# Performance work log

Hardware: AMD Instinct MI355X
Metric: run time of the kernel (lower is better)

## Reference

```python
import jax, jax.numpy as jnp
import numpy as np

E, D, H, B, S = 16, 1024, 256, 4, 4096  # num_splats, model_dim, ff_dim//num_splats, batch, seq_len


def setup_inputs() -> dict:
    key = jax.random.key(0)
    ks = jax.random.split(key, 8)
    s = 0.02  # init scale for stability
    return {
        "x": jax.random.normal(ks[0], (B, S, D), dtype=jnp.float32),
        "splat_id": jax.random.randint(ks[1], (S,), 0, E, dtype=jnp.int32),
        "W1": jax.random.normal(ks[2], (E, D, H), dtype=jnp.float32) * s,
        "b1": jnp.zeros((E, H), dtype=jnp.float32),
        "W2": jax.random.normal(ks[3], (E, H, D), dtype=jnp.float32) * s,
        "b2": jnp.zeros((E, D), dtype=jnp.float32),
        "Wg1": jax.random.normal(ks[4], (D, D), dtype=jnp.float32) * s,
        "bg1": jnp.zeros((D,), dtype=jnp.float32),
        "Wg2": jax.random.normal(ks[5], (D, D), dtype=jnp.float32) * s,
        "bg2": jnp.zeros((D,), dtype=jnp.float32),
    }


def reference(x, splat_id, W1, b1, W2, b2, Wg1, bg1, Wg2, bg2):
    # Splat-aware dispatch: token s is processed by expert splat_id[s].
    # Equivalent vectorized form: run every expert's small MLP, mask at the
    # hidden layer by expert assignment, and sum over experts (each token is
    # assigned to exactly one expert, matching the gather->MLP->scatter loop).
    nE = W1.shape[0]
    onehot = (splat_id[None, :] == jnp.arange(nE, dtype=splat_id.dtype)[:, None]).astype(x.dtype)  # [E,S]
    # hidden: [E,B,S,H]
    h = jax.nn.gelu(jnp.einsum('bsd,edh->ebsh', x, W1) + b1[:, None, None, :], approximate=False)
    h = h * onehot[:, None, :, None]  # zero tokens not routed to expert e
    routed = jnp.einsum('ebsh,ehd->bsd', h, W2)  # [B,S,D]
    routed = routed + jnp.einsum('es,ed->sd', onehot, b2)[None, :, :]  # per-token expert bias
    # global aggregator MLP (torch GELU default = exact erf form)
    g = jax.nn.gelu(routed @ Wg1 + bg1, approximate=False)
    return g @ Wg2 + bg2
```

## Files before the change

kernel.cpp:

```cpp
#include <hip/hip_runtime.h>


#define DEV __device__ __forceinline__

typedef float f32x4 __attribute__((ext_vector_type(4)));
typedef short short8 __attribute__((ext_vector_type(8)));

DEV unsigned short f2bf(float f) {
  unsigned u = __float_as_uint(f);
  u += 0x7fffu + ((u >> 16) & 1u);
  return (unsigned short)(u >> 16);
}

DEV void gload_lds16(const void* g, void* l) {
  __builtin_amdgcn_global_load_lds(
      (const __attribute__((address_space(1))) unsigned int*)g,
      (__attribute__((address_space(3))) unsigned int*)l, 16, 0, 0);
}

DEV float gelu_exact(float v) {
  return 0.5f * v * (1.0f + erff(v * 0.70710678118654752f));
}

#define BARRIER() __builtin_amdgcn_s_barrier()
#define VMW(n)    asm volatile("s_waitcnt vmcnt(" #n ")" ::: "memory")

__global__ __launch_bounds__(256) void cast_bf16_kernel(
    const float* __restrict__ in, unsigned short* __restrict__ out, long n) {
  long i = ((long)blockIdx.x * 256 + threadIdx.x) * 8;
  if (i >= n) return;
  float4 v0 = *(const float4*)(in + i);
  float4 v1 = *(const float4*)(in + i + 4);
  uint4 o;
  o.x = (unsigned)f2bf(v0.x) | ((unsigned)f2bf(v0.y) << 16);
  o.y = (unsigned)f2bf(v0.z) | ((unsigned)f2bf(v0.w) << 16);
  o.z = (unsigned)f2bf(v1.x) | ((unsigned)f2bf(v1.y) << 16);
  o.w = (unsigned)f2bf(v1.z) | ((unsigned)f2bf(v1.w) << 16);
  *(uint4*)(out + i) = o;
}

__global__ __launch_bounds__(256) void tcast_kernel(
    const float* __restrict__ in, unsigned short* __restrict__ out,
    int R, int C, long stride) {
  __shared__ float tile[64][65];
  const int t = threadIdx.x;
  const long base = (long)blockIdx.z * stride;
  const int r0 = blockIdx.y * 64, c0 = blockIdx.x * 64;
  const int cc = t & 63, rr = t >> 6;
#pragma unroll
  for (int i = 0; i < 16; i++) {
    int r = rr + i * 4;
    tile[r][cc] = in[base + (long)(r0 + r) * C + (c0 + cc)];
  }
  __syncthreads();
#pragma unroll
  for (int i = 0; i < 16; i++) {
    int c = rr + i * 4;
    out[base + (long)(c0 + c) * R + (r0 + cc)] = f2bf(tile[cc][c]);
  }
}

__global__ __launch_bounds__(256) void route_kernel(
    const int* __restrict__ sid, int S, int* __restrict__ offs, int* __restrict__ order) {
  __shared__ int cnt[16], cur[16];
  const int t = threadIdx.x;
  if (t < 16) cnt[t] = 0;
  __syncthreads();
  for (int s = t; s < S; s += 256) atomicAdd(&cnt[sid[s]], 1);
  __syncthreads();
  if (t == 0) {
    int a = 0;
    for (int e = 0; e < 16; e++) { offs[e] = a; cur[e] = a; a += cnt[e]; }
    offs[16] = a;
  }
  __syncthreads();
  for (int s = t; s < S; s += 256) {
    int p = atomicAdd(&cur[sid[s]], 1);
    order[p] = s;
  }
}

template <bool GATHER_A, bool SCATTER_C, bool GELU, bool OUT_F32>
__global__ __launch_bounds__(256) void gemm_mfma(
    const unsigned short* __restrict__ A, const unsigned short* __restrict__ BT,
    const float* __restrict__ bias, void* __restrict__ Cout,
    int M, int N, int K,
    const int* __restrict__ order, const int* __restrict__ offs,
    int S, long btStride, int biasStride) {
  const int t = (int)threadIdx.x;
  const int lane = t & 63;
  const int w = t >> 6;
  const int wm = w >> 1, wn = w & 1;
  const int tileN = (int)blockIdx.x, tileM = (int)blockIdx.y, e = (int)blockIdx.z;

  const int o0 = offs[e], o1 = offs[e + 1];
  const int rowBase = 4 * o0;
  const int Me = 4 * (o1 - o0);
  if (tileM * 128 >= Me) return;
  const unsigned short* bt = BT + (long)e * btStride;
  const float* bs = bias + (long)e * biasStride;

  __shared__ __align__(16) unsigned short lA[128 * 64];
  __shared__ __align__(16) unsigned short lB[128 * 64];

  const unsigned short* aSrc[4];
  const unsigned short* bSrc[4];
  {
    const int q = t & 7;
#pragma unroll
    for (int i = 0; i < 4; i++) {
      const int row = i * 32 + (t >> 3);
      const int koff = ((q * 16) ^ ((row & 7) << 4)) >> 1;
      long arow;
      const int lrow = tileM * 128 + row;
      const int rr = (lrow < Me) ? lrow : (Me - 1);
      const int g = rowBase + rr;
      if (GATHER_A) {
        const int s = order[g >> 2];
        arow = (long)(g & 3) * S + s;
      } else {
        arow = g;
      }
      aSrc[i] = A + arow * (long)K + koff;
      const int col = tileN * 128 + row;
      bSrc[i] = bt + (long)col * K + koff;
    }
  }

  f32x4 acc[4][4] = {};

  const int KT = K >> 6;
  for (int kt = 0; kt < KT; kt++) {
    __syncthreads();
#pragma unroll
    for (int i = 0; i < 4; i++) {
      gload_lds16(aSrc[i] + (kt << 6), (void*)(lA + i * 2048 + w * 512));
      gload_lds16(bSrc[i] + (kt << 6), (void*)(lB + i * 2048 + w * 512));
    }
    __syncthreads();
#pragma unroll
    for (int kk = 0; kk < 2; kk++) {
      short8 af[4], bfr[4];
      const int kbyte = kk * 64 + (lane >> 4) * 16;
#pragma unroll
      for (int mi = 0; mi < 4; mi++) {
        const int row = wm * 64 + mi * 16 + (lane & 15);
        const int off = row * 128 + (kbyte ^ ((row & 7) << 4));
        af[mi] = *(const short8*)((const char*)lA + off);
      }
#pragma unroll
      for (int ni = 0; ni < 4; ni++) {
        const int row = wn * 64 + ni * 16 + (lane & 15);
        const int off = row * 128 + (kbyte ^ ((row & 7) << 4));
        bfr[ni] = *(const short8*)((const char*)lB + off);
      }
#pragma unroll
      for (int mi = 0; mi < 4; mi++)
#pragma unroll
        for (int ni = 0; ni < 4; ni++)
          acc[mi][ni] = __builtin_amdgcn_mfma_f32_16x16x32_bf16(af[mi], bfr[ni], acc[mi][ni], 0, 0, 0);
    }
  }

  float bcol[4];
#pragma unroll
  for (int ni = 0; ni < 4; ni++)
    bcol[ni] = bs[tileN * 128 + wn * 64 + ni * 16 + (lane & 15)];

#pragma unroll
  for (int mi = 0; mi < 4; mi++) {
#pragma unroll
    for (int j = 0; j < 4; j++) {
      const int lrow = tileM * 128 + wm * 64 + mi * 16 + ((lane >> 4) * 4) + j;
      if (lrow >= Me) continue;
      const int g = rowBase + lrow;
      long crow;
      if (SCATTER_C) crow = (long)(g & 3) * S + order[g >> 2];
      else crow = g;
#pragma unroll
      for (int ni = 0; ni < 4; ni++) {
        float v = acc[mi][ni][j] + bcol[ni];
        if (GELU) v = gelu_exact(v);
        const long cidx = crow * (long)N + tileN * 128 + wn * 64 + ni * 16 + (lane & 15);
        if (OUT_F32) ((float*)Cout)[cidx] = v;
        else ((unsigned short*)Cout)[cidx] = f2bf(v);
      }
    }
  }
}

template <bool GELU, bool OUT_F32>
__global__ __launch_bounds__(512, 2) void gemm_8phase(
    const unsigned short* __restrict__ A, const unsigned short* __restrict__ BT,
    const float* __restrict__ bias, void* __restrict__ Cout,
    int N, int K, int ntiles) {
  __shared__ __align__(16) unsigned short lds[8 * 8192];

  const int t = (int)threadIdx.x;
  const int lane = t & 63;
  const int w = t >> 6;
  const int wm = w >> 2;
  const int wn = w & 3;

  const int cpx = (int)gridDim.x >> 3;
  const int swz = ((int)blockIdx.x & 7) * cpx + ((int)blockIdx.x >> 3);
  const int mtile = swz / ntiles, ntile = swz % ntiles;

  const int tq = t & 7;
  const unsigned short* srcA[2][2];
  const unsigned short* srcB[2][2];
#pragma unroll
  for (int i = 0; i < 2; i++) {
    const int ir = i * 64 + (t >> 3);
    const int koffE = ((tq * 16) ^ ((ir & 7) << 4)) >> 1;
#pragma unroll
    for (int h = 0; h < 2; h++) {
      const int ra = (ir & 63) + (h << 6) + ((ir >> 6) << 7);
      srcA[i][h] = A + (long)(mtile * 256 + ra) * K + koffE;
      const int cb = (ir & 31) + (h << 5) + ((ir >> 5) << 6);
      srcB[i][h] = BT + (long)(ntile * 256 + cb) * K + koffE;
    }
  }
  const int dstE = (t >> 3) * 64 + tq * 8;

  auto STAGE = [&](int d, int mat, int h, int kt) {
    unsigned short* dst = lds + ((d * 4 + mat * 2 + h) << 13) + dstE;
    const unsigned short* s0 = (mat == 0 ? srcA[0][h] : srcB[0][h]) + (kt << 6);
    const unsigned short* s1 = (mat == 0 ? srcA[1][h] : srcB[1][h]) + (kt << 6);
    gload_lds16(s0, dst);
    gload_lds16(s1, dst + 4096);
  };

  short8 aReg[8], bReg[8];
  const int klane = (lane >> 4) << 4;
  const int rsw = (lane & 7) << 4;

  auto LDA = [&](int d, int mh) {
    const char* base = (const char*)(lds + ((d * 4 + mh) << 13));
    const int r0 = wm * 64 + (lane & 15);
#pragma unroll
    for (int m = 0; m < 4; m++) {
      const int row = r0 + m * 16;
#pragma unroll
      for (int kk = 0; kk < 2; kk++)
        aReg[m * 2 + kk] = *(const short8*)(base + row * 128 + ((kk * 64 + klane) ^ rsw));
    }
  };
  auto LDB = [&](int d, int nh) {
    const char* base = (const char*)(lds + ((d * 4 + 2 + nh) << 13));
    const int r0 = wn * 32 + (lane & 15);
#pragma unroll
    for (int n = 0; n < 2; n++) {
      const int row = r0 + n * 16;
#pragma unroll
      for (int kk = 0; kk < 2; kk++)
        bReg[(nh * 2 + n) * 2 + kk] = *(const short8*)(base + row * 128 + ((kk * 64 + klane) ^ rsw));
    }
  };

  f32x4 acc[8][4] = {};
  auto MMA = [&](int mb, int nb) {
    __builtin_amdgcn_s_setprio(1);
#pragma unroll
    for (int kk = 0; kk < 2; kk++)
#pragma unroll
      for (int m = 0; m < 4; m++)
#pragma unroll
        for (int n = 0; n < 2; n++)
          acc[mb + m][nb + n] = __builtin_amdgcn_mfma_f32_16x16x32_bf16(
              aReg[m * 2 + kk], bReg[(nb + n) * 2 + kk], acc[mb + m][nb + n], 0, 0, 0);
    __builtin_amdgcn_s_setprio(0);
  };

  const int KT = K >> 6;

  {
    const int t1 = (KT > 1) ? 1 : 0;
    STAGE(0, 0, 0, 0); STAGE(0, 1, 0, 0); STAGE(0, 1, 1, 0); STAGE(0, 0, 1, 0);
    STAGE(1, 0, 0, t1); STAGE(1, 1, 0, t1); STAGE(1, 1, 1, t1);
    VMW(6);
    BARRIER();
  }

  for (int it = 0; it < (KT >> 1); ++it) {
    const int tb = (2 * it + 1 < KT) ? 2 * it + 1 : KT - 1;
    int nx = 2 * it + 2; if (nx >= KT) nx = KT - 1;
    int ny = 2 * it + 3; if (ny >= KT) ny = KT - 1;
    LDA(0, 0); LDB(0, 0); STAGE(1, 0, 1, tb);
    BARRIER();
    MMA(0, 0);
    BARRIER();
    LDB(0, 1); STAGE(0, 0, 0, nx);
    BARRIER();
    MMA(0, 2);
    BARRIER();
    LDA(0, 1); STAGE(0, 1, 0, nx);
    BARRIER();
    MMA(4, 0);
    BARRIER();
    STAGE(0, 1, 1, nx);
    BARRIER();
    MMA(4, 2);
    VMW(6);
    BARRIER();
    LDA(1, 0); LDB(1, 0); STAGE(0, 0, 1, nx);
    BARRIER();
    MMA(0, 0);
    BARRIER();
    LDB(1, 1); STAGE(1, 0, 0, ny);
    BARRIER();
    MMA(0, 2);
    BARRIER();
    LDA(1, 1); STAGE(1, 1, 0, ny);
    BARRIER();
    MMA(4, 0);
    BARRIER();
    STAGE(1, 1, 1, ny);
    BARRIER();
    MMA(4, 2);
    VMW(6);
    BARRIER();
  }
  VMW(0);

  float bcol[4];
#pragma unroll
  for (int n = 0; n < 4; n++)
    bcol[n] = bias[ntile * 256 + wn * 64 + n * 16 + (lane & 15)];
  const int cbase = ntile * 256 + wn * 64 + (lane & 15);
#pragma unroll
  for (int m = 0; m < 8; m++) {
#pragma unroll
    for (int j = 0; j < 4; j++) {
      const long crow = mtile * 256 + wm * 128 + m * 16 + ((lane >> 4) << 2) + j;
#pragma unroll
      for (int n = 0; n < 4; n++) {
        float v = acc[m][n][j] + bcol[n];
        if (GELU) v = gelu_exact(v);
        const long cidx = crow * (long)N + cbase + n * 16;
        if (OUT_F32) ((float*)Cout)[cidx] = v;
        else ((unsigned short*)Cout)[cidx] = f2bf(v);
      }
    }
  }
}

extern "C" void kernel_launch(void* const* d_in, const int* in_sizes, int n_in,
                              void* d_out, int out_size, void* d_ws, size_t ws_size,
                              hipStream_t stream) {
  const float* x   = (const float*)d_in[0];
  const int*   sid = (const int*)d_in[1];
  const float* W1  = (const float*)d_in[2];
  const float* b1  = (const float*)d_in[3];
  const float* W2  = (const float*)d_in[4];
  const float* b2  = (const float*)d_in[5];
  const float* Wg1 = (const float*)d_in[6];
  const float* bg1 = (const float*)d_in[7];
  const float* Wg2 = (const float*)d_in[8];
  const float* bg2 = (const float*)d_in[9];
  (void)in_sizes; (void)n_in; (void)out_size; (void)ws_size;

  constexpr int E = 16, D = 1024, H = 256, S = 4096, B = 4;
  constexpr long NT = (long)B * S;

  char* ws = (char*)d_ws;
  unsigned short* xb   = (unsigned short*)(ws);
  unsigned short* w1t  = (unsigned short*)(ws + 33554432);
  unsigned short* w2t  = (unsigned short*)(ws + 41943040);
  unsigned short* wg1t = (unsigned short*)(ws + 50331648);
  unsigned short* wg2t = (unsigned short*)(ws + 52428800);
  unsigned short* hbuf = (unsigned short*)(ws + 54525952);
  unsigned short* rout = (unsigned short*)(ws + 62914560);
  int* offs  = (int*)(ws + 96468992);
  int* order = (int*)(ws + 96469248);

  cast_bf16_kernel<<<dim3((unsigned)(NT * D / 2048)), 256, 0, stream>>>(x, xb, NT * D);
  tcast_kernel<<<dim3(H / 64, D / 64, E), 256, 0, stream>>>(W1, w1t, D, H, (long)D * H);
  tcast_kernel<<<dim3(D / 64, H / 64, E), 256, 0, stream>>>(W2, w2t, H, D, (long)D * H);
  tcast_kernel<<<dim3(D / 64, D / 64, 1), 256, 0, stream>>>(Wg1, wg1t, D, D, (long)D * D);
  tcast_kernel<<<dim3(D / 64, D / 64, 1), 256, 0, stream>>>(Wg2, wg2t, D, D, (long)D * D);
  route_kernel<<<1, 256, 0, stream>>>(sid, S, offs, order);

  gemm_mfma<true, false, true, false><<<dim3(H / 128, 128, E), 256, 0, stream>>>(
      xb, w1t, b1, hbuf, (int)NT, H, D, order, offs, S, (long)H * D, H);
  gemm_mfma<false, true, false, false><<<dim3(D / 128, 128, E), 256, 0, stream>>>(
      hbuf, w2t, b2, rout, (int)NT, D, H, order, offs, S, (long)D * H, D);
  gemm_8phase<true, false><<<dim3((unsigned)(NT / 256) * (D / 256)), 512, 0, stream>>>(
      rout, wg1t, bg1, xb, D, D, D / 256);
  gemm_8phase<false, true><<<dim3((unsigned)(NT / 256) * (D / 256)), 512, 0, stream>>>(
      xb, wg2t, bg2, d_out, D, D, D / 256);
}
```

Measured before the change: 196.4 us.

## Fuse prep casts, compact expert tile list, switch dense GEMMs to 32x32 MFMA

The five cast/transpose launches become one prep kernel that picks its work by block index. The route kernel now also builds a compact list of (expert, row-base) tiles, so the grouped GEMMs launch 144 tiles instead of 128x16 mostly-empty blocks. The dense aggregator GEMMs switch from 16x16x32 to 32x32x16 bf16 MFMA, with matching LDS fragment loads and epilogue indexing, to cut LDS reads per FLOP. The 144-tile cap assumes expert counts stay close to uniform, and the new accumulator layout changes register pressure.

```diff
diff --git a/kernel.cpp b/kernel.cpp
--- a/kernel.cpp
+++ b/kernel.cpp
@@ -4,6 +4,7 @@
 #define DEV __device__ __forceinline__
 
 typedef float f32x4 __attribute__((ext_vector_type(4)));
+typedef float f32x16 __attribute__((ext_vector_type(16)));
 typedef short short8 __attribute__((ext_vector_type(8)));
 
 DEV unsigned short f2bf(float f) {
@@ -25,27 +26,48 @@
 #define BARRIER() __builtin_amdgcn_s_barrier()
 #define VMW(n)    asm volatile("s_waitcnt vmcnt(" #n ")" ::: "memory")
 
-__global__ __launch_bounds__(256) void cast_bf16_kernel(
-    const float* __restrict__ in, unsigned short* __restrict__ out, long n) {
-  long i = ((long)blockIdx.x * 256 + threadIdx.x) * 8;
-  if (i >= n) return;
-  float4 v0 = *(const float4*)(in + i);
-  float4 v1 = *(const float4*)(in + i + 4);
-  uint4 o;
-  o.x = (unsigned)f2bf(v0.x) | ((unsigned)f2bf(v0.y) << 16);
-  o.y = (unsigned)f2bf(v0.z) | ((unsigned)f2bf(v0.w) << 16);
-  o.z = (unsigned)f2bf(v1.x) | ((unsigned)f2bf(v1.y) << 16);
-  o.w = (unsigned)f2bf(v1.z) | ((unsigned)f2bf(v1.w) << 16);
-  *(uint4*)(out + i) = o;
-}
-
-__global__ __launch_bounds__(256) void tcast_kernel(
-    const float* __restrict__ in, unsigned short* __restrict__ out,
-    int R, int C, long stride) {
+__global__ __launch_bounds__(256) void prep_kernel(
+    const float* __restrict__ x, unsigned short* __restrict__ xb,
+    const float* __restrict__ W1, unsigned short* __restrict__ w1t,
+    const float* __restrict__ W2, unsigned short* __restrict__ w2t,
+    const float* __restrict__ Wg1, unsigned short* __restrict__ wg1t,
+    const float* __restrict__ Wg2, unsigned short* __restrict__ wg2t) {
   __shared__ float tile[64][65];
   const int t = threadIdx.x;
-  const long base = (long)blockIdx.z * stride;
-  const int r0 = blockIdx.y * 64, c0 = blockIdx.x * 64;
+  int id = (int)blockIdx.x;
+  if (id < 8192) {
+    long i = ((long)id * 256 + t) * 8;
+    float4 v0 = *(const float4*)(x + i);
+    float4 v1 = *(const float4*)(x + i + 4);
+    uint4 o;
+    o.x = (unsigned)f2bf(v0.x) | ((unsigned)f2bf(v0.y) << 16);
+    o.y = (unsigned)f2bf(v0.z) | ((unsigned)f2bf(v0.w) << 16);
+    o.z = (unsigned)f2bf(v1.x) | ((unsigned)f2bf(v1.y) << 16);
+    o.w = (unsigned)f2bf(v1.z) | ((unsigned)f2bf(v1.w) << 16);
+    *(uint4*)(xb + i) = o;
+    return;
+  }
+  id -= 8192;
+  const float* in; unsigned short* out;
+  int R, C, r0, c0; long base;
+  if (id < 1024) {
+    in = W1; out = w1t; R = 1024; C = 256;
+    base = (long)(id >> 6) * 262144;
+    r0 = ((id >> 2) & 15) * 64; c0 = (id & 3) * 64;
+  } else if (id < 2048) {
+    id -= 1024;
+    in = W2; out = w2t; R = 256; C = 1024;
+    base = (long)(id >> 6) * 262144;
+    r0 = ((id >> 4) & 3) * 64; c0 = (id & 15) * 64;
+  } else if (id < 2304) {
+    id -= 2048;
+    in = Wg1; out = wg1t; R = 1024; C = 1024; base = 0;
+    r0 = (id >> 4) * 64; c0 = (id & 15) * 64;
+  } else {
+    id -= 2304;
+    in = Wg2; out = wg2t; R = 1024; C = 1024; base = 0;
+    r0 = (id >> 4) * 64; c0 = (id & 15) * 64;
+  }
   const int cc = t & 63, rr = t >> 6;
 #pragma unroll
   for (int i = 0; i < 16; i++) {
@@ -61,7 +83,8 @@
 }
 
 __global__ __launch_bounds__(256) void route_kernel(
-    const int* __restrict__ sid, int S, int* __restrict__ offs, int* __restrict__ order) {
+    const int* __restrict__ sid, int S, int* __restrict__ offs, int* __restrict__ order,
+    int* __restrict__ tileE, int* __restrict__ tileR, int* __restrict__ ntl) {
   __shared__ int cnt[16], cur[16];
   const int t = threadIdx.x;
   if (t < 16) cnt[t] = 0;
@@ -72,6 +95,16 @@
     int a = 0;
     for (int e = 0; e < 16; e++) { offs[e] = a; cur[e] = a; a += cnt[e]; }
     offs[16] = a;
+    int nt = 0;
+    for (int e = 0; e < 16; e++) {
+      const int rows = 4 * cnt[e];
+      for (int r = 0; r < rows; r += 128) {
+        tileE[nt] = e;
+        tileR[nt] = 4 * offs[e] + r;
+        nt++;
+      }
+    }
+    ntl[0] = nt;
   }
   __syncthreads();
   for (int s = t; s < S; s += 256) {
@@ -84,19 +117,23 @@
 __global__ __launch_bounds__(256) void gemm_mfma(
     const unsigned short* __restrict__ A, const unsigned short* __restrict__ BT,
     const float* __restrict__ bias, void* __restrict__ Cout,
-    int M, int N, int K,
+    int N, int K,
     const int* __restrict__ order, const int* __restrict__ offs,
+    const int* __restrict__ tileE, const int* __restrict__ tileR,
+    const int* __restrict__ ntl,
     int S, long btStride, int biasStride) {
+  const int ti = (int)blockIdx.y;
+  if (ti >= ntl[0]) return;
   const int t = (int)threadIdx.x;
   const int lane = t & 63;
   const int w = t >> 6;
   const int wm = w >> 1, wn = w & 1;
-  const int tileN = (int)blockIdx.x, tileM = (int)blockIdx.y, e = (int)blockIdx.z;
-
-  const int o0 = offs[e], o1 = offs[e + 1];
-  const int rowBase = 4 * o0;
-  const int Me = 4 * (o1 - o0);
-  if (tileM * 128 >= Me) return;
+  const int tileN = (int)blockIdx.x;
+
+  const int e = tileE[ti];
+  const int rowBase = tileR[ti];
+  int Me = 4 * offs[e + 1] - rowBase;
+  if (Me > 128) Me = 128;
   const unsigned short* bt = BT + (long)e * btStride;
   const float* bs = bias + (long)e * biasStride;
 
@@ -111,10 +148,9 @@
     for (int i = 0; i < 4; i++) {
       const int row = i * 32 + (t >> 3);
       const int koff = ((q * 16) ^ ((row & 7) << 4)) >> 1;
+      const int rr = (row < Me) ? row : (Me - 1);
+      const int g = rowBase + rr;
       long arow;
-      const int lrow = tileM * 128 + row;
-      const int rr = (lrow < Me) ? lrow : (Me - 1);
-      const int g = rowBase + rr;
       if (GATHER_A) {
         const int s = order[g >> 2];
         arow = (long)(g & 3) * S + s;
@@ -171,7 +207,7 @@
   for (int mi = 0; mi < 4; mi++) {
 #pragma unroll
     for (int j = 0; j < 4; j++) {
-      const int lrow = tileM * 128 + wm * 64 + mi * 16 + ((lane >> 4) * 4) + j;
+      const int lrow = wm * 64 + mi * 16 + ((lane >> 4) * 4) + j;
       if (lrow >= Me) continue;
       const int g = rowBase + lrow;
       long crow;
@@ -190,7 +226,7 @@
 }
 
 template <bool GELU, bool OUT_F32>
-__global__ __launch_bounds__(512, 2) void gemm_8phase(
+__global__ __launch_bounds__(512, 2) void gemm_8p32(
     const unsigned short* __restrict__ A, const unsigned short* __restrict__ BT,
     const float* __restrict__ bias, void* __restrict__ Cout,
     int N, int K, int ntiles) {
@@ -231,44 +267,40 @@
     gload_lds16(s1, dst + 4096);
   };
 
-  short8 aReg[8], bReg[8];
-  const int klane = (lane >> 4) << 4;
-  const int rsw = (lane & 7) << 4;
+  short8 aR[2][4], bR[2][4];
+  const int kcol = ((lane >> 5) << 4);
+  const int l31 = lane & 31;
 
   auto LDA = [&](int d, int mh) {
     const char* base = (const char*)(lds + ((d * 4 + mh) << 13));
-    const int r0 = wm * 64 + (lane & 15);
-#pragma unroll
-    for (int m = 0; m < 4; m++) {
-      const int row = r0 + m * 16;
-#pragma unroll
-      for (int kk = 0; kk < 2; kk++)
-        aReg[m * 2 + kk] = *(const short8*)(base + row * 128 + ((kk * 64 + klane) ^ rsw));
+    const int r0 = wm * 64 + l31;
+#pragma unroll
+    for (int m = 0; m < 2; m++) {
+      const int row = r0 + m * 32;
+      const int rs = (row & 7) << 4;
+#pragma unroll
+      for (int kk = 0; kk < 4; kk++)
+        aR[m][kk] = *(const short8*)(base + row * 128 + ((kk * 32 + kcol) ^ rs));
     }
   };
   auto LDB = [&](int d, int nh) {
     const char* base = (const char*)(lds + ((d * 4 + 2 + nh) << 13));
-    const int r0 = wn * 32 + (lane & 15);
-#pragma unroll
-    for (int n = 0; n < 2; n++) {
-      const int row = r0 + n * 16;
-#pragma unroll
-      for (int kk = 0; kk < 2; kk++)
-        bReg[(nh * 2 + n) * 2 + kk] = *(const short8*)(base + row * 128 + ((kk * 64 + klane) ^ rsw));
-    }
+    const int col = wn * 32 + l31;
+    const int rs = (col & 7) << 4;
+#pragma unroll
+    for (int kk = 0; kk < 4; kk++)
+      bR[nh][kk] = *(const short8*)(base + col * 128 + ((kk * 32 + kcol) ^ rs));
   };
 
-  f32x4 acc[8][4] = {};
-  auto MMA = [&](int mb, int nb) {
+  f32x16 acc[4][2] = {};
+  auto MMA = [&](int mh, int nh) {
     __builtin_amdgcn_s_setprio(1);
 #pragma unroll
-    for (int kk = 0; kk < 2; kk++)
-#pragma unroll
-      for (int m = 0; m < 4; m++)
-#pragma unroll
-        for (int n = 0; n < 2; n++)
-          acc[mb + m][nb + n] = __builtin_amdgcn_mfma_f32_16x16x32_bf16(
-              aReg[m * 2 + kk], bReg[(nb + n) * 2 + kk], acc[mb + m][nb + n], 0, 0, 0);
+    for (int kk = 0; kk < 4; kk++)
+#pragma unroll
+      for (int m = 0; m < 2; m++)
+        acc[mh * 2 + m][nh] = __builtin_amdgcn_mfma_f32_32x32x16_bf16(
+            aR[m][kk], bR[nh][kk], acc[mh * 2 + m][nh], 0, 0, 0);
     __builtin_amdgcn_s_setprio(0);
   };
 
@@ -292,15 +324,15 @@
     BARRIER();
     LDB(0, 1); STAGE(0, 0, 0, nx);
     BARRIER();
-    MMA(0, 2);
+    MMA(0, 1);
     BARRIER();
     LDA(0, 1); STAGE(0, 1, 0, nx);
     BARRIER();
-    MMA(4, 0);
+    MMA(1, 0);
     BARRIER();
     STAGE(0, 1, 1, nx);
     BARRIER();
-    MMA(4, 2);
+    MMA(1, 1);
     VMW(6);
     BARRIER();
     LDA(1, 0); LDB(1, 0); STAGE(0, 0, 1, nx);
@@ -309,35 +341,36 @@
     BARRIER();
     LDB(1, 1); STAGE(1, 0, 0, ny);
     BARRIER();
-    MMA(0, 2);
+    MMA(0, 1);
     BARRIER();
     LDA(1, 1); STAGE(1, 1, 0, ny);
     BARRIER();
-    MMA(4, 0);
+    MMA(1, 0);
     BARRIER();
     STAGE(1, 1, 1, ny);
     BARRIER();
-    MMA(4, 2);
+    MMA(1, 1);
     VMW(6);
     BARRIER();
   }
   VMW(0);
 
-  float bcol[4];
-#pragma unroll
-  for (int n = 0; n < 4; n++)
-    bcol[n] = bias[ntile * 256 + wn * 64 + n * 16 + (lane & 15)];
-  const int cbase = ntile * 256 + wn * 64 + (lane & 15);
-#pragma unroll
-  for (int m = 0; m < 8; m++) {
-#pragma unroll
-    for (int j = 0; j < 4; j++) {
-      const long crow = mtile * 256 + wm * 128 + m * 16 + ((lane >> 4) << 2) + j;
-#pragma unroll
-      for (int n = 0; n < 4; n++) {
-        float v = acc[m][n][j] + bcol[n];
+  float bc[2];
+#pragma unroll
+  for (int n = 0; n < 2; n++)
+    bc[n] = bias[ntile * 256 + wn * 64 + n * 32 + l31];
+  const int cbase = ntile * 256 + wn * 64 + l31;
+  const int rbase = mtile * 256 + wm * 128 + ((lane >> 5) << 2);
+#pragma unroll
+  for (int mf = 0; mf < 4; mf++) {
+#pragma unroll
+    for (int reg = 0; reg < 16; reg++) {
+      const long crow = rbase + mf * 32 + (reg & 3) + ((reg >> 2) << 3);
+#pragma unroll
+      for (int nf = 0; nf < 2; nf++) {
+        float v = acc[mf][nf][reg] + bc[nf];
         if (GELU) v = gelu_exact(v);
-        const long cidx = crow * (long)N + cbase + n * 16;
+        const long cidx = crow * (long)N + cbase + nf * 32;
         if (OUT_F32) ((float*)Cout)[cidx] = v;
         else ((unsigned short*)Cout)[cidx] = f2bf(v);
       }
@@ -360,7 +393,7 @@
   const float* bg2 = (const float*)d_in[9];
   (void)in_sizes; (void)n_in; (void)out_size; (void)ws_size;
 
-  constexpr int E = 16, D = 1024, H = 256, S = 4096, B = 4;
+  constexpr int D = 1024, H = 256, S = 4096, B = 4;
   constexpr long NT = (long)B * S;
 
   char* ws = (char*)d_ws;
@@ -373,20 +406,19 @@
   unsigned short* rout = (unsigned short*)(ws + 62914560);
   int* offs  = (int*)(ws + 96468992);
   int* order = (int*)(ws + 96469248);
-
-  cast_bf16_kernel<<<dim3((unsigned)(NT * D / 2048)), 256, 0, stream>>>(x, xb, NT * D);
-  tcast_kernel<<<dim3(H / 64, D / 64, E), 256, 0, stream>>>(W1, w1t, D, H, (long)D * H);
-  tcast_kernel<<<dim3(D / 64, H / 64, E), 256, 0, stream>>>(W2, w2t, H, D, (long)D * H);
-  tcast_kernel<<<dim3(D / 64, D / 64, 1), 256, 0, stream>>>(Wg1, wg1t, D, D, (long)D * D);
-  tcast_kernel<<<dim3(D / 64, D / 64, 1), 256, 0, stream>>>(Wg2, wg2t, D, D, (long)D * D);
-  route_kernel<<<1, 256, 0, stream>>>(sid, S, offs, order);
-
-  gemm_mfma<true, false, true, false><<<dim3(H / 128, 128, E), 256, 0, stream>>>(
-      xb, w1t, b1, hbuf, (int)NT, H, D, order, offs, S, (long)H * D, H);
-  gemm_mfma<false, true, false, false><<<dim3(D / 128, 128, E), 256, 0, stream>>>(
-      hbuf, w2t, b2, rout, (int)NT, D, H, order, offs, S, (long)D * H, D);
-  gemm_8phase<true, false><<<dim3((unsigned)(NT / 256) * (D / 256)), 512, 0, stream>>>(
+  int* tileE = (int*)(ws + 96485632);
+  int* tileR = (int*)(ws + 96486208);
+  int* ntl   = (int*)(ws + 96486784);
+
+  prep_kernel<<<dim3(10752), 256, 0, stream>>>(x, xb, W1, w1t, W2, w2t, Wg1, wg1t, Wg2, wg2t);
+  route_kernel<<<1, 256, 0, stream>>>(sid, S, offs, order, tileE, tileR, ntl);
+
+  gemm_mfma<true, false, true, false><<<dim3(H / 128, 144), 256, 0, stream>>>(
+      xb, w1t, b1, hbuf, H, D, order, offs, tileE, tileR, ntl, S, (long)H * D, H);
+  gemm_mfma<false, true, false, false><<<dim3(D / 128, 144), 256, 0, stream>>>(
+      hbuf, w2t, b2, rout, D, H, order, offs, tileE, tileR, ntl, S, (long)D * H, D);
+  gemm_8p32<true, false><<<dim3((unsigned)(NT / 256) * (D / 256)), 512, 0, stream>>>(
       rout, wg1t, bg1, xb, D, D, D / 256);
-  gemm_8phase<false, true><<<dim3((unsigned)(NT / 256) * (D / 256)), 512, 0, stream>>>(
+  gemm_8p32<false, true><<<dim3((unsigned)(NT / 256) * (D / 256)), 512, 0, stream>>>(
       xb, wg2t, bg2, d_out, D, D, D / 256);
 }
```

Result: no change. 194.6 us (-0.9%).

## Fuse expert MLP into one kernel, merge weight casts, add double-buffered aggregator GEMM

Applied to the files above, without the earlier changes.

Merges the four weight transpose-cast launches into one prep kernel and drops the separate fp32-to-bf16 cast of x, which is now converted inside the expert kernel while gathering rows. The two expert GEMMs become one kernel: each block takes a 64-row tile of one expert from a tile list built by the router, keeps the GELU hidden activations in LDS and immediately applies W2. This removes the hidden buffer round trip through global memory and the blocks that previously exited early. The first aggregator GEMM moves to a new double-buffered 256x256 kernel with one block per CU. The costs are lower tile efficiency in the fused kernel (64-row tiles, W2 re-staged per block) and a fixed grid of 272 blocks sized to the worst-case tile count.

```diff
diff --git a/kernel.cpp b/kernel.cpp
--- a/kernel.cpp
+++ b/kernel.cpp
@@ -12,7 +12,7 @@
   return (unsigned short)(u >> 16);
 }
 
-DEV void gload_lds16(const void* g, void* l) {
+DEV void gload16(const void* g, void* l) {
   __builtin_amdgcn_global_load_lds(
       (const __attribute__((address_space(1))) unsigned int*)g,
       (__attribute__((address_space(3))) unsigned int*)l, 16, 0, 0);
@@ -25,27 +25,34 @@
 #define BARRIER() __builtin_amdgcn_s_barrier()
 #define VMW(n)    asm volatile("s_waitcnt vmcnt(" #n ")" ::: "memory")
 
-__global__ __launch_bounds__(256) void cast_bf16_kernel(
-    const float* __restrict__ in, unsigned short* __restrict__ out, long n) {
-  long i = ((long)blockIdx.x * 256 + threadIdx.x) * 8;
-  if (i >= n) return;
-  float4 v0 = *(const float4*)(in + i);
-  float4 v1 = *(const float4*)(in + i + 4);
-  uint4 o;
-  o.x = (unsigned)f2bf(v0.x) | ((unsigned)f2bf(v0.y) << 16);
-  o.y = (unsigned)f2bf(v0.z) | ((unsigned)f2bf(v0.w) << 16);
-  o.z = (unsigned)f2bf(v1.x) | ((unsigned)f2bf(v1.y) << 16);
-  o.w = (unsigned)f2bf(v1.z) | ((unsigned)f2bf(v1.w) << 16);
-  *(uint4*)(out + i) = o;
-}
-
-__global__ __launch_bounds__(256) void tcast_kernel(
-    const float* __restrict__ in, unsigned short* __restrict__ out,
-    int R, int C, long stride) {
+__global__ __launch_bounds__(256) void prep_kernel(
+    const float* __restrict__ W1, unsigned short* __restrict__ w1t,
+    const float* __restrict__ W2, unsigned short* __restrict__ w2t,
+    const float* __restrict__ Wg1, unsigned short* __restrict__ wg1t,
+    const float* __restrict__ Wg2, unsigned short* __restrict__ wg2t) {
   __shared__ float tile[64][65];
   const int t = threadIdx.x;
-  const long base = (long)blockIdx.z * stride;
-  const int r0 = blockIdx.y * 64, c0 = blockIdx.x * 64;
+  int id = (int)blockIdx.x;
+  const float* in; unsigned short* out;
+  int R, C, r0, c0; long base;
+  if (id < 1024) {
+    in = W1; out = w1t; R = 1024; C = 256;
+    base = (long)(id >> 6) * 262144;
+    r0 = ((id >> 2) & 15) * 64; c0 = (id & 3) * 64;
+  } else if (id < 2048) {
+    id -= 1024;
+    in = W2; out = w2t; R = 256; C = 1024;
+    base = (long)(id >> 6) * 262144;
+    r0 = ((id >> 4) & 3) * 64; c0 = (id & 15) * 64;
+  } else if (id < 2304) {
+    id -= 2048;
+    in = Wg1; out = wg1t; R = 1024; C = 1024; base = 0;
+    r0 = (id >> 4) * 64; c0 = (id & 15) * 64;
+  } else {
+    id -= 2304;
+    in = Wg2; out = wg2t; R = 1024; C = 1024; base = 0;
+    r0 = (id >> 4) * 64; c0 = (id & 15) * 64;
+  }
   const int cc = t & 63, rr = t >> 6;
 #pragma unroll
   for (int i = 0; i < 16; i++) {
@@ -61,7 +68,8 @@
 }
 
 __global__ __launch_bounds__(256) void route_kernel(
-    const int* __restrict__ sid, int S, int* __restrict__ offs, int* __restrict__ order) {
+    const int* __restrict__ sid, int S, int* __restrict__ offs, int* __restrict__ order,
+    int* __restrict__ tileE, int* __restrict__ tileR, int* __restrict__ ntl) {
   __shared__ int cnt[16], cur[16];
   const int t = threadIdx.x;
   if (t < 16) cnt[t] = 0;
@@ -72,6 +80,16 @@
     int a = 0;
     for (int e = 0; e < 16; e++) { offs[e] = a; cur[e] = a; a += cnt[e]; }
     offs[16] = a;
+    int nt = 0;
+    for (int e = 0; e < 16; e++) {
+      const int rows = 4 * cnt[e];
+      for (int r = 0; r < rows; r += 64) {
+        tileE[nt] = e;
+        tileR[nt] = 4 * offs[e] + r;
+        nt++;
+      }
+    }
+    ntl[0] = nt;
   }
   __syncthreads();
   for (int s = t; s < S; s += 256) {
@@ -80,108 +98,251 @@
   }
 }
 
-template <bool GATHER_A, bool SCATTER_C, bool GELU, bool OUT_F32>
-__global__ __launch_bounds__(256) void gemm_mfma(
-    const unsigned short* __restrict__ A, const unsigned short* __restrict__ BT,
-    const float* __restrict__ bias, void* __restrict__ Cout,
-    int M, int N, int K,
+__global__ __launch_bounds__(512, 2) void fused_expert(
+    const float* __restrict__ x,
+    const unsigned short* __restrict__ w1t, const float* __restrict__ b1,
+    const unsigned short* __restrict__ w2t, const float* __restrict__ b2,
+    unsigned short* __restrict__ rout,
     const int* __restrict__ order, const int* __restrict__ offs,
-    int S, long btStride, int biasStride) {
+    const int* __restrict__ tileE, const int* __restrict__ tileR,
+    const int* __restrict__ ntl) {
+  constexpr int S = 4096, D = 1024, H = 256;
+  const int ti = (int)blockIdx.x;
+  if (ti >= ntl[0]) return;
+
+  __shared__ __align__(16) unsigned short lA[64 * 64];
+  __shared__ __align__(16) unsigned short lB[256 * 64];
+  __shared__ __align__(16) unsigned short hS[64 * 256];
+
   const int t = (int)threadIdx.x;
   const int lane = t & 63;
   const int w = t >> 6;
-  const int wm = w >> 1, wn = w & 1;
-  const int tileN = (int)blockIdx.x, tileM = (int)blockIdx.y, e = (int)blockIdx.z;
-
-  const int o0 = offs[e], o1 = offs[e + 1];
-  const int rowBase = 4 * o0;
-  const int Me = 4 * (o1 - o0);
-  if (tileM * 128 >= Me) return;
-  const unsigned short* bt = BT + (long)e * btStride;
-  const float* bs = bias + (long)e * biasStride;
-
-  __shared__ __align__(16) unsigned short lA[128 * 64];
-  __shared__ __align__(16) unsigned short lB[128 * 64];
-
-  const unsigned short* aSrc[4];
-  const unsigned short* bSrc[4];
-  {
-    const int q = t & 7;
-#pragma unroll
-    for (int i = 0; i < 4; i++) {
-      const int row = i * 32 + (t >> 3);
-      const int koff = ((q * 16) ^ ((row & 7) << 4)) >> 1;
-      long arow;
-      const int lrow = tileM * 128 + row;
-      const int rr = (lrow < Me) ? lrow : (Me - 1);
-      const int g = rowBase + rr;
-      if (GATHER_A) {
-        const int s = order[g >> 2];
-        arow = (long)(g & 3) * S + s;
-      } else {
-        arow = g;
-      }
-      aSrc[i] = A + arow * (long)K + koff;
-      const int col = tileN * 128 + row;
-      bSrc[i] = bt + (long)col * K + koff;
-    }
-  }
-
-  f32x4 acc[4][4] = {};
-
-  const int KT = K >> 6;
-  for (int kt = 0; kt < KT; kt++) {
+  const int wm = w >> 2;
+  const int wn = w & 3;
+
+  const int e = tileE[ti];
+  const int rowBase = tileR[ti];
+  int Me = 4 * offs[e + 1] - rowBase;
+  if (Me > 64) Me = 64;
+
+  const int ar = t >> 3;
+  const int arr = (ar < Me) ? ar : (Me - 1);
+  const int ga = rowBase + arr;
+  const float* xsrc = x + ((long)(ga & 3) * S + order[ga >> 2]) * D + (t & 7) * 8;
+  unsigned short* aDst = lA + ar * 64 + (((((t & 7) * 16)) ^ ((ar & 7) << 4)) >> 1);
+
+  const unsigned short* b1src[4];
+#pragma unroll
+  for (int i = 0; i < 4; i++) {
+    const int row = i * 64 + (t >> 3);
+    b1src[i] = w1t + (long)e * H * D + (long)row * D + ((((t & 7) * 16) ^ ((row & 7) << 4)) >> 1);
+  }
+  const int dstE = (t >> 3) * 64 + (t & 7) * 8;
+
+  f32x4 acc[2][4] = {};
+  float4 xv0 = *(const float4*)(xsrc);
+  float4 xv1 = *(const float4*)(xsrc + 4);
+
+  for (int kt = 0; kt < 16; kt++) {
     __syncthreads();
-#pragma unroll
-    for (int i = 0; i < 4; i++) {
-      gload_lds16(aSrc[i] + (kt << 6), (void*)(lA + i * 2048 + w * 512));
-      gload_lds16(bSrc[i] + (kt << 6), (void*)(lB + i * 2048 + w * 512));
+    short8 av;
+    av[0] = (short)f2bf(xv0.x); av[1] = (short)f2bf(xv0.y);
+    av[2] = (short)f2bf(xv0.z); av[3] = (short)f2bf(xv0.w);
+    av[4] = (short)f2bf(xv1.x); av[5] = (short)f2bf(xv1.y);
+    av[6] = (short)f2bf(xv1.z); av[7] = (short)f2bf(xv1.w);
+    *(short8*)aDst = av;
+#pragma unroll
+    for (int i = 0; i < 4; i++) gload16(b1src[i] + (kt << 6), lB + i * 4096 + dstE);
+    if (kt < 15) {
+      xv0 = *(const float4*)(xsrc + (kt + 1) * 64);
+      xv1 = *(const float4*)(xsrc + (kt + 1) * 64 + 4);
     }
     __syncthreads();
 #pragma unroll
     for (int kk = 0; kk < 2; kk++) {
-      short8 af[4], bfr[4];
-      const int kbyte = kk * 64 + (lane >> 4) * 16;
-#pragma unroll
-      for (int mi = 0; mi < 4; mi++) {
-        const int row = wm * 64 + mi * 16 + (lane & 15);
-        const int off = row * 128 + (kbyte ^ ((row & 7) << 4));
-        af[mi] = *(const short8*)((const char*)lA + off);
+      short8 aF[2], bF[4];
+      const int kb = kk * 64 + ((lane >> 4) << 4);
+#pragma unroll
+      for (int mi = 0; mi < 2; mi++) {
+        const int row = wm * 32 + mi * 16 + (lane & 15);
+        aF[mi] = *(const short8*)((const char*)lA + row * 128 + (kb ^ ((row & 7) << 4)));
       }
 #pragma unroll
       for (int ni = 0; ni < 4; ni++) {
         const int row = wn * 64 + ni * 16 + (lane & 15);
-        const int off = row * 128 + (kbyte ^ ((row & 7) << 4));
-        bfr[ni] = *(const short8*)((const char*)lB + off);
-      }
-#pragma unroll
-      for (int mi = 0; mi < 4; mi++)
+        bF[ni] = *(const short8*)((const char*)lB + row * 128 + (kb ^ ((row & 7) << 4)));
+      }
+#pragma unroll
+      for (int mi = 0; mi < 2; mi++)
 #pragma unroll
         for (int ni = 0; ni < 4; ni++)
-          acc[mi][ni] = __builtin_amdgcn_mfma_f32_16x16x32_bf16(af[mi], bfr[ni], acc[mi][ni], 0, 0, 0);
-    }
+          acc[mi][ni] = __builtin_amdgcn_mfma_f32_16x16x32_bf16(aF[mi], bF[ni], acc[mi][ni], 0, 0, 0);
+    }
+  }
+
+  {
+    float bc[4];
+#pragma unroll
+    for (int ni = 0; ni < 4; ni++)
+      bc[ni] = b1[e * H + wn * 64 + ni * 16 + (lane & 15)];
+#pragma unroll
+    for (int mi = 0; mi < 2; mi++)
+#pragma unroll
+      for (int j = 0; j < 4; j++) {
+        const int crow = wm * 32 + mi * 16 + ((lane >> 4) << 2) + j;
+#pragma unroll
+        for (int ni = 0; ni < 4; ni++) {
+          const int ccol = wn * 64 + ni * 16 + (lane & 15);
+          const float v = gelu_exact(acc[mi][ni][j] + bc[ni]);
+          hS[crow * 256 + (((ccol * 2) ^ ((crow & 7) << 4)) >> 1)] = f2bf(v);
+        }
+      }
+  }
+  __syncthreads();
+
+  const unsigned short* b2base = w2t + (long)e * D * H;
+  for (int nc = 0; nc < 8; nc++) {
+    f32x4 a2[2][2] = {};
+    for (int ks = 0; ks < 4; ks++) {
+      __syncthreads();
+#pragma unroll
+      for (int i = 0; i < 2; i++) {
+        const int row = i * 64 + (t >> 3);
+        const unsigned short* src = b2base + (long)(nc * 128 + row) * H + (ks << 6) +
+                                    ((((t & 7) * 16) ^ ((row & 7) << 4)) >> 1);
+        gload16(src, lB + i * 4096 + dstE);
+      }
+      __syncthreads();
+#pragma unroll
+      for (int kk = 0; kk < 2; kk++) {
+        short8 aF[2], bF[2];
+        const int kbh = ks * 128 + kk * 64 + ((lane >> 4) << 4);
+        const int kb = kk * 64 + ((lane >> 4) << 4);
+#pragma unroll
+        for (int mi = 0; mi < 2; mi++) {
+          const int row = wm * 32 + mi * 16 + (lane & 15);
+          aF[mi] = *(const short8*)((const char*)hS + row * 512 + (kbh ^ ((row & 7) << 4)));
+        }
+#pragma unroll
+        for (int ni = 0; ni < 2; ni++) {
+          const int row = wn * 32 + ni * 16 + (lane & 15);
+          bF[ni] = *(const short8*)((const char*)lB + row * 128 + (kb ^ ((row & 7) << 4)));
+        }
+#pragma unroll
+        for (int mi = 0; mi < 2; mi++)
+#pragma unroll
+          for (int ni = 0; ni < 2; ni++)
+            a2[mi][ni] = __builtin_amdgcn_mfma_f32_16x16x32_bf16(aF[mi], bF[ni], a2[mi][ni], 0, 0, 0);
+      }
+    }
+    float bc2[2];
+#pragma unroll
+    for (int ni = 0; ni < 2; ni++)
+      bc2[ni] = b2[e * D + nc * 128 + wn * 32 + ni * 16 + (lane & 15)];
+#pragma unroll
+    for (int mi = 0; mi < 2; mi++)
+#pragma unroll
+      for (int j = 0; j < 4; j++) {
+        const int lrow = wm * 32 + mi * 16 + ((lane >> 4) << 2) + j;
+        if (lrow >= Me) continue;
+        const int g = rowBase + lrow;
+        const long crow = (long)(g & 3) * S + order[g >> 2];
+#pragma unroll
+        for (int ni = 0; ni < 2; ni++) {
+          const float v = a2[mi][ni][j] + bc2[ni];
+          rout[crow * D + nc * 128 + wn * 32 + ni * 16 + (lane & 15)] = f2bf(v);
+        }
+      }
+  }
+}
+
+template <bool GELU, bool OUT_F32>
+__global__ __launch_bounds__(512, 1) void gemm_2ph(
+    const unsigned short* __restrict__ A, const unsigned short* __restrict__ BT,
+    const float* __restrict__ bias, void* __restrict__ Cout,
+    int N, int K, int ntiles) {
+  __shared__ __align__(16) unsigned short lds[2][2][256 * 64];
+
+  const int t = (int)threadIdx.x;
+  const int lane = t & 63;
+  const int w = t >> 6;
+  const int wm = w >> 2;
+  const int wn = w & 3;
+
+  const int cpx = (int)gridDim.x >> 3;
+  const int swz = ((int)blockIdx.x & 7) * cpx + ((int)blockIdx.x >> 3);
+  const int mtile = swz / ntiles, ntile = swz % ntiles;
+
+  const int tq = t & 7;
+  const unsigned short* srcA[4];
+  const unsigned short* srcB[4];
+#pragma unroll
+  for (int i = 0; i < 4; i++) {
+    const int row = i * 64 + (t >> 3);
+    const int koffE = ((tq * 16) ^ ((row & 7) << 4)) >> 1;
+    srcA[i] = A + (long)(mtile * 256 + row) * K + koffE;
+    srcB[i] = BT + (long)(ntile * 256 + row) * K + koffE;
+  }
+  const int dstE = (t >> 3) * 64 + tq * 8;
+
+  auto STAGE = [&](int buf, int kt) {
+    const long ko = (long)kt << 6;
+#pragma unroll
+    for (int i = 0; i < 4; i++) gload16(srcA[i] + ko, &lds[buf][0][i * 4096 + dstE]);
+#pragma unroll
+    for (int i = 0; i < 4; i++) gload16(srcB[i] + ko, &lds[buf][1][i * 4096 + dstE]);
+  };
+
+  f32x4 acc[8][4] = {};
+  const int KT = K >> 6;
+
+  STAGE(0, 0);
+  __syncthreads();
+
+  int buf = 0;
+  for (int kt = 0; kt < KT; kt++) {
+    if (kt + 1 < KT) STAGE(buf ^ 1, kt + 1);
+#pragma unroll
+    for (int kk = 0; kk < 2; kk++) {
+      short8 aF[8], bF[4];
+      const int kb = kk * 64 + ((lane >> 4) << 4);
+#pragma unroll
+      for (int m = 0; m < 8; m++) {
+        const int row = wm * 128 + m * 16 + (lane & 15);
+        aF[m] = *(const short8*)((const char*)&lds[buf][0][0] + row * 128 + (kb ^ ((row & 7) << 4)));
+      }
+#pragma unroll
+      for (int n = 0; n < 4; n++) {
+        const int row = wn * 64 + n * 16 + (lane & 15);
+        bF[n] = *(const short8*)((const char*)&lds[buf][1][0] + row * 128 + (kb ^ ((row & 7) << 4)));
+      }
+      __builtin_amdgcn_s_setprio(1);
+#pragma unroll
+      for (int m = 0; m < 8; m++)
+#pragma unroll
+        for (int n = 0; n < 4; n++)
+          acc[m][n] = __builtin_amdgcn_mfma_f32_16x16x32_bf16(aF[m], bF[n], acc[m][n], 0, 0, 0);
+      __builtin_amdgcn_s_setprio(0);
+    }
+    __syncthreads();
+    buf ^= 1;
   }
 
   float bcol[4];
 #pragma unroll
-  for (int ni = 0; ni < 4; ni++)
-    bcol[ni] = bs[tileN * 128 + wn * 64 + ni * 16 + (lane & 15)];
-
-#pragma unroll
-  for (int mi = 0; mi < 4; mi++) {
+  for (int n = 0; n < 4; n++)
+    bcol[n] = bias[ntile * 256 + wn * 64 + n * 16 + (lane & 15)];
+  const int cbase = ntile * 256 + wn * 64 + (lane & 15);
+#pragma unroll
+  for (int m = 0; m < 8; m++) {
 #pragma unroll
     for (int j = 0; j < 4; j++) {
-      const int lrow = tileM * 128 + wm * 64 + mi * 16 + ((lane >> 4) * 4) + j;
-      if (lrow >= Me) continue;
-      const int g = rowBase + lrow;
-      long crow;
-      if (SCATTER_C) crow = (long)(g & 3) * S + order[g >> 2];
-      else crow = g;
-#pragma unroll
-      for (int ni = 0; ni < 4; ni++) {
-        float v = acc[mi][ni][j] + bcol[ni];
+      const long crow = mtile * 256 + wm * 128 + m * 16 + ((lane >> 4) << 2) + j;
+#pragma unroll
+      for (int n = 0; n < 4; n++) {
+        float v = acc[m][n][j] + bcol[n];
         if (GELU) v = gelu_exact(v);
-        const long cidx = crow * (long)N + tileN * 128 + wn * 64 + ni * 16 + (lane & 15);
+        const long cidx = crow * (long)N + cbase + n * 16;
         if (OUT_F32) ((float*)Cout)[cidx] = v;
         else ((unsigned short*)Cout)[cidx] = f2bf(v);
       }
@@ -227,8 +388,8 @@
     unsigned short* dst = lds + ((d * 4 + mat * 2 + h) << 13) + dstE;
     const unsigned short* s0 = (mat == 0 ? srcA[0][h] : srcB[0][h]) + (kt << 6);
     const unsigned short* s1 = (mat == 0 ? srcA[1][h] : srcB[1][h]) + (kt << 6);
-    gload_lds16(s0, dst);
-    gload_lds16(s1, dst + 4096);
+    gload16(s0, dst);
+    gload16(s1, dst + 4096);
   };
 
   short8 aReg[8], bReg[8];
@@ -360,33 +521,30 @@
   const float* bg2 = (const float*)d_in[9];
   (void)in_sizes; (void)n_in; (void)out_size; (void)ws_size;
 
-  constexpr int E = 16, D = 1024, H = 256, S = 4096, B = 4;
+  constexpr int D = 1024, S = 4096, B = 4;
   constexpr long NT = (long)B * S;
 
   char* ws = (char*)d_ws;
-  unsigned short* xb   = (unsigned short*)(ws);
+  unsigned short* g    = (unsigned short*)(ws);
   unsigned short* w1t  = (unsigned short*)(ws + 33554432);
   unsigned short* w2t  = (unsigned short*)(ws + 41943040);
   unsigned short* wg1t = (unsigned short*)(ws + 50331648);
   unsigned short* wg2t = (unsigned short*)(ws + 52428800);
-  unsigned short* hbuf = (unsigned short*)(ws + 54525952);
   unsigned short* rout = (unsigned short*)(ws + 62914560);
   int* offs  = (int*)(ws + 96468992);
   int* order = (int*)(ws + 96469248);
-
-  cast_bf16_kernel<<<dim3((unsigned)(NT * D / 2048)), 256, 0, stream>>>(x, xb, NT * D);
-  tcast_kernel<<<dim3(H / 64, D / 64, E), 256, 0, stream>>>(W1, w1t, D, H, (long)D * H);
-  tcast_kernel<<<dim3(D / 64, H / 64, E), 256, 0, stream>>>(W2, w2t, H, D, (long)D * H);
-  tcast_kernel<<<dim3(D / 64, D / 64, 1), 256, 0, stream>>>(Wg1, wg1t, D, D, (long)D * D);
-  tcast_kernel<<<dim3(D / 64, D / 64, 1), 256, 0, stream>>>(Wg2, wg2t, D, D, (long)D * D);
-  route_kernel<<<1, 256, 0, stream>>>(sid, S, offs, order);
-
-  gemm_mfma<true, false, true, false><<<dim3(H / 128, 128, E), 256, 0, stream>>>(
-      xb, w1t, b1, hbuf, (int)NT, H, D, order, offs, S, (long)H * D, H);
-  gemm_mfma<false, true, false, false><<<dim3(D / 128, 128, E), 256, 0, stream>>>(
-      hbuf, w2t, b2, rout, (int)NT, D, H, order, offs, S, (long)D * H, D);
-  gemm_8phase<true, false><<<dim3((unsigned)(NT / 256) * (D / 256)), 512, 0, stream>>>(
-      rout, wg1t, bg1, xb, D, D, D / 256);
+  int* tileE = (int*)(ws + 96485632);
+  int* tileR = (int*)(ws + 96486912);
+  int* ntl   = (int*)(ws + 96488192);
+
+  prep_kernel<<<dim3(2560), 256, 0, stream>>>(W1, w1t, W2, w2t, Wg1, wg1t, Wg2, wg2t);
+  route_kernel<<<1, 256, 0, stream>>>(sid, S, offs, order, tileE, tileR, ntl);
+
+  fused_expert<<<dim3(272), 512, 0, stream>>>(
+      x, w1t, b1, w2t, b2, rout, order, offs, tileE, tileR, ntl);
+
+  gemm_2ph<true, false><<<dim3((unsigned)(NT / 256) * (D / 256)), 512, 0, stream>>>(
+      rout, wg1t, bg1, g, D, D, D / 256);
   gemm_8phase<false, true><<<dim3((unsigned)(NT / 256) * (D / 256)), 512, 0, stream>>>(
-      xb, wg2t, bg2, d_out, D, D, D / 256);
-}
+      g, wg2t, bg2, d_out, D, D, D / 256);
+}
```

After: 182.0 us. 1.08x faster.
